# Kernel optimization log

Hardware: AMD Instinct MI355X
Metric: run time of the kernel (lower is better)

The kernel has to match this reference:

```python
import jax, jax.numpy as jnp
import numpy as np

# ---- static configuration (mirrors pdf.__init__ on a BaTiO3 system) ----
B, N = 2, 1024          # frames, atoms
NBINS = 100
R0, R1 = 0.5, 7.5       # r_range
CUTOFF = R1 + 0.5       # cutoff_boundary
L = 24.0                # cubic cell edge
PI = np.pi

# unique atomic numbers of BaTiO3, sorted (as __init__ computes from system.numbers)
UNIQUE_Z = [8, 22, 56]
ATOM_PAIRS = [(8, 8), (8, 22), (8, 56), (22, 22), (22, 56), (56, 56)]
_PAIR_COEFFI = {(82,82):125.44,(82,22):98.56,(82,8):107.52,(82,40):98.56,(56,56):125.44,
                (56,22):98.56,(56,8):107.52,(56,40):98.56,(22,22):19.36,(22,8):42.24,
                (22,40):19.36,(40,40):19.36,(40,8):42.24,(40,22):19.36,(8,8):23.04}
COEFFS = np.array([_PAIR_COEFFI.get(p, _PAIR_COEFFI.get((p[1], p[0]), 1.0))
                   for p in ATOM_PAIRS], dtype=np.float32)          # [T]
PAIR_KEYS = np.array([min(p)*1000 + max(p) for p in ATOM_PAIRS], dtype=np.int32)  # [T]

# static upper-triangular pair indices (i < j), as generate_nbr_list enumerates pairs once
I_IDX, J_IDX = np.triu_indices(N, k=1)   # each [P], P = N(N-1)/2


def setup_inputs() -> dict:
    key = jax.random.key(0)
    k1, _ = jax.random.split(key)
    xyz = jax.random.uniform(k1, (B, N, 3), dtype=jnp.float32) * L
    # BaTiO3 composition 1:1:3
    numbers = np.concatenate([np.full(205, 56), np.full(205, 22), np.full(614, 8)])
    rng = np.random.default_rng(0)
    rng.shuffle(numbers)
    bins = jnp.linspace(R0, R1, NBINS + 1, dtype=jnp.float32)
    cell = jnp.full((3,), L, dtype=jnp.float32)
    return {"xyz": xyz, "numbers": jnp.asarray(numbers, dtype=jnp.int32),
            "bins": bins, "cell": cell}


def reference(xyz, numbers, bins, cell):
    # per-pair unordered type key: min(z_i,z_j)*1000 + max(z_i,z_j)
    zi = numbers[I_IDX]
    zj = numbers[J_IDX]
    pair_key = jnp.minimum(zi, zj) * 1000 + jnp.maximum(zi, zj)          # [P]
    type_sel = (pair_key[None, :] == jnp.asarray(PAIR_KEYS)[:, None])    # [T, P] bool

    centers = 0.5 * (bins[:-1] + bins[1:])                               # [nbins]
    width = bins[1] - bins[0]
    sigma = width / np.sqrt(2.0 * PI)
    vol_bins = (4.0 * PI / 3.0) * (bins[1:] ** 3 - bins[:-1] ** 3)       # [nbins]
    V = (4.0 / 3.0) * PI * R1 ** 3
    coeffs = jnp.asarray(COEFFS)                                         # [T]

    def frame_pdf(x):                                                    # x: [N,3]
        d = x[I_IDX] - x[J_IDX]                                          # [P,3]
        d = d - cell * jnp.round(d / cell)                               # minimum image (diag cell)
        dist = jnp.sqrt(jnp.sum(d * d, axis=-1))                         # [P]
        within = dist < CUTOFF                                           # neighbor-list cutoff
        # Gaussian soft histogram kernel over all candidate pairs
        K = jnp.exp(-0.5 * ((dist[:, None] - centers[None, :]) / sigma) ** 2)  # [P,nbins]
        sel = (type_sel & within[None, :]).astype(K.dtype)               # [T,P]
        counts = sel @ K                                                 # [T,nbins]
        counts = counts / counts.sum(axis=-1, keepdims=True)
        rdf = counts / (vol_bins / V)[None, :]
        return jnp.sum(coeffs[:, None] * (rdf - 1.0), axis=0)            # [nbins]

    pdf_l = jax.vmap(frame_pdf)(xyz)                                     # [B,nbins]
    pdf_average = jnp.mean(pdf_l, axis=0) / 416.16
    return pdf_average, bins
```

## Files before the change

kernel.cpp:

```cpp
#include <hip/hip_runtime.h>
#include <math.h>

#define NBINS   100
#define NTYPES  6
#define NHIST   (NTYPES * NBINS)
#define NATOMS  1024
#define OPB     4
#define GPB     128
#define T1      1024
#define NW1     (T1 / 64)
#define R0f     0.5f
#define R1f     7.5f

__global__ __launch_bounds__(T1)
void pdf_pairs_rot(const float* __restrict__ xyz,
                   const int*   __restrict__ numbers,
                   const float* __restrict__ bins,
                   const float* __restrict__ cell,
                   float* __restrict__ partial,
                   float* __restrict__ out,
                   int out_size) {
    __shared__ float shist[NW1][NHIST];

    const int frame = blockIdx.y;
    const int tid   = threadIdx.x;
    const int wave  = tid >> 6;

    if (blockIdx.x == 0 && blockIdx.y == 0) {
        if (tid < NBINS) out[tid] = 0.0f;
        if (out_size >= NBINS + (NBINS + 1) && tid >= NBINS && tid < 2 * NBINS + 1)
            out[tid] = bins[tid - NBINS];
    }

    for (int k = tid; k < NW1 * NHIST; k += T1)
        ((float*)shist)[k] = 0.0f;

    const float* fx = xyz + (size_t)frame * NATOMS * 3;
    const float xi = fx[tid * 3 + 0];
    const float yi = fx[tid * 3 + 1];
    const float zi = fx[tid * 3 + 2];
    const int   zn = numbers[tid];
    const int   ti = (zn > 21) ? ((zn > 55) ? 2 : 1) : 0;

    const float cx = cell[0], cy = cell[1], cz = cell[2];
    const float icx = 1.0f / cx, icy = 1.0f / cy, icz = 1.0f / cz;
    const float w     = bins[1] - bins[0];
    const float sigma = w * 0.3989422804014327f;
    const float negc  = -(0.5f / (sigma * sigma)) * 1.4426950408889634f;
    const float invw  = 1.0f / w;
    const float w05   = 0.5f * w;
    const float c1    = -2.0f * negc * w;
    const float c2    = negc * w * w;

    __syncthreads();

    float* wh = shist[wave];

    #pragma unroll
    for (int q = 0; q < OPB; ++q) {
        const int o = blockIdx.x * OPB + 1 + q;
        const int j = (tid + o) & (NATOMS - 1);
        if (o == NATOMS / 2 && tid >= NATOMS / 2) continue;

        const float xj = fx[j * 3 + 0];
        const float yj = fx[j * 3 + 1];
        const float zj = fx[j * 3 + 2];
        const int   zjn = numbers[j];
        const int   tj = (zjn > 21) ? ((zjn > 55) ? 2 : 1) : 0;

        float dx = xi - xj;
        float dy = yi - yj;
        float dz = zi - zj;
        dx -= cx * rintf(dx * icx);
        dy -= cy * rintf(dy * icy);
        dz -= cz * rintf(dz * icz);
        const float dist = sqrtf(dx * dx + dy * dy + dz * dz);

        const int lo = min(ti, tj);
        const int hi = max(ti, tj);
        const int t  = 2 * lo - (lo >> 1) + hi;
        float* th = wh + t * NBINS;

        const float t0 = dist - R0f;
        const float kf = floorf(t0 * invw);
        const int   kc = (int)kf;
        const float base = (t0 - w05) - kf * w;
        const float A  = negc * base * base;
        const float Bq = c1 * base;

        #pragma unroll
        for (int u = 0; u < 5; ++u) {
            const float m = (float)(u - 2);
            const int   k = kc + (u - 2);
            const float arg = (A + m * m * c2) + m * Bq;
            const float v = __builtin_amdgcn_exp2f(arg);
            if ((unsigned)k < (unsigned)NBINS)
                atomicAdd(&th[k], v);
        }
    }
    __syncthreads();

    float* gp = partial + ((size_t)frame * GPB + blockIdx.x) * NHIST;
    for (int k = tid; k < NHIST; k += T1) {
        float v = 0.0f;
        #pragma unroll
        for (int wv = 0; wv < NW1; ++wv) v += shist[wv][k];
        gp[k] = v;
    }
}

__global__ __launch_bounds__(256)
void pdf_finish(const float* __restrict__ partial,
                const float* __restrict__ bins,
                float* __restrict__ out,
                int nframes) {
    __shared__ float wred[4];
    const int t   = blockIdx.x;
    const int b   = blockIdx.y;
    const int tid = threadIdx.x;

    float row = 0.0f;
    if (tid < NBINS) {
        const float* base = partial + (size_t)b * GPB * NHIST + t * NBINS + tid;
        #pragma unroll 8
        for (int g = 0; g < GPB; ++g)
            row += base[(size_t)g * NHIST];
    }

    float v = (tid < NBINS) ? row : 0.0f;
    #pragma unroll
    for (int off = 32; off > 0; off >>= 1) v += __shfl_down(v, off, 64);
    if ((tid & 63) == 0) wred[tid >> 6] = v;
    __syncthreads();
    const float ssum = (wred[0] + wred[1]) + (wred[2] + wred[3]);

    if (tid < NBINS) {
        const float PI = 3.14159265358979323846f;
        const float V = (4.0f / 3.0f) * PI * R1f * R1f * R1f;
        const float coeffs[NTYPES] = {23.04f, 42.24f, 107.52f, 19.36f, 98.56f, 125.44f};
        const float b0 = bins[tid], b1 = bins[tid + 1];
        const float volb = (4.0f * PI / 3.0f) * (b1 * b1 * b1 - b0 * b0 * b0);
        const float scale = V / volb;
        const float contrib = coeffs[t] * (row / ssum * scale - 1.0f)
                              / (float)nframes / 416.16f;
        unsafeAtomicAdd(&out[tid], contrib);
    }
}

extern "C" void kernel_launch(void* const* d_in, const int* in_sizes, int n_in,
                              void* d_out, int out_size, void* d_ws, size_t ws_size,
                              hipStream_t stream) {
    const float* xyz     = (const float*)d_in[0];
    const int*   numbers = (const int*)d_in[1];
    const float* bins    = (const float*)d_in[2];
    const float* cell    = (const float*)d_in[3];
    float* out     = (float*)d_out;
    float* partial = (float*)d_ws;

    const int B = in_sizes[0] / (NATOMS * 3);

    dim3 gridA(GPB, B);
    pdf_pairs_rot<<<gridA, T1, 0, stream>>>(xyz, numbers, bins, cell,
                                            partial, out, out_size);
    dim3 gridB(NTYPES, B);
    pdf_finish<<<gridB, 256, 0, stream>>>(partial, bins, out, B);
}
```

Before: 18.53 us.

## Halve block size with two atoms per thread, vectorize LDS, parallelize finish reduction

The pair kernel now uses 512-thread blocks, with each thread handling two i-atoms. The grid doubles to 256 blocks per frame with 2 offsets each, which halves the per-block LDS histogram footprint and raises the block count. Zeroing and reducing the LDS histograms now use float4 accesses. The finish kernel spreads the 256-partial sum over 1024 threads in 8 groups, then combines them through shared memory. The partial buffer gets twice as many rows, so there is more global write and read traffic in exchange for more parallelism.

```diff
diff --git a/kernel.cpp b/kernel.cpp
--- a/kernel.cpp
+++ b/kernel.cpp
@@ -5,9 +5,9 @@
 #define NTYPES  6
 #define NHIST   (NTYPES * NBINS)
 #define NATOMS  1024
-#define OPB     4
-#define GPB     128
-#define T1      1024
+#define OPB     2
+#define GPB     256
+#define T1      512
 #define NW1     (T1 / 64)
 #define R0f     0.5f
 #define R1f     7.5f
@@ -22,25 +22,29 @@
                    int out_size) {
     __shared__ float shist[NW1][NHIST];
 
-    const int frame = blockIdx.y;
     const int tid   = threadIdx.x;
     const int wave  = tid >> 6;
+    const int frame = blockIdx.y;
 
     if (blockIdx.x == 0 && blockIdx.y == 0) {
         if (tid < NBINS) out[tid] = 0.0f;
-        if (out_size >= NBINS + (NBINS + 1) && tid >= NBINS && tid < 2 * NBINS + 1)
+        if (out_size >= 2 * NBINS + 1 && tid >= NBINS && tid < 2 * NBINS + 1)
             out[tid] = bins[tid - NBINS];
     }
 
-    for (int k = tid; k < NW1 * NHIST; k += T1)
-        ((float*)shist)[k] = 0.0f;
+    {
+        float4* z = (float4*)&shist[0][0];
+        for (int v = tid; v < NW1 * NHIST / 4; v += T1)
+            z[v] = make_float4(0.f, 0.f, 0.f, 0.f);
+    }
 
     const float* fx = xyz + (size_t)frame * NATOMS * 3;
-    const float xi = fx[tid * 3 + 0];
-    const float yi = fx[tid * 3 + 1];
-    const float zi = fx[tid * 3 + 2];
-    const int   zn = numbers[tid];
-    const int   ti = (zn > 21) ? ((zn > 55) ? 2 : 1) : 0;
+    const int i0 = tid, i1 = tid + T1;
+    const float x0 = fx[i0 * 3 + 0], y0 = fx[i0 * 3 + 1], z0 = fx[i0 * 3 + 2];
+    const float x1 = fx[i1 * 3 + 0], y1 = fx[i1 * 3 + 1], z1 = fx[i1 * 3 + 2];
+    const int   zn0 = numbers[i0], zn1 = numbers[i1];
+    const int   t0i = (zn0 > 21) ? ((zn0 > 55) ? 2 : 1) : 0;
+    const int   t1i = (zn1 > 21) ? ((zn1 > 55) ? 2 : 1) : 0;
 
     const float cx = cell[0], cy = cell[1], cz = cell[2];
     const float icx = 1.0f / cx, icy = 1.0f / cy, icz = 1.0f / cz;
@@ -59,72 +63,96 @@
     #pragma unroll
     for (int q = 0; q < OPB; ++q) {
         const int o = blockIdx.x * OPB + 1 + q;
-        const int j = (tid + o) & (NATOMS - 1);
-        if (o == NATOMS / 2 && tid >= NATOMS / 2) continue;
-
-        const float xj = fx[j * 3 + 0];
-        const float yj = fx[j * 3 + 1];
-        const float zj = fx[j * 3 + 2];
-        const int   zjn = numbers[j];
-        const int   tj = (zjn > 21) ? ((zjn > 55) ? 2 : 1) : 0;
-
-        float dx = xi - xj;
-        float dy = yi - yj;
-        float dz = zi - zj;
-        dx -= cx * rintf(dx * icx);
-        dy -= cy * rintf(dy * icy);
-        dz -= cz * rintf(dz * icz);
-        const float dist = sqrtf(dx * dx + dy * dy + dz * dz);
-
-        const int lo = min(ti, tj);
-        const int hi = max(ti, tj);
-        const int t  = 2 * lo - (lo >> 1) + hi;
-        float* th = wh + t * NBINS;
-
-        const float t0 = dist - R0f;
-        const float kf = floorf(t0 * invw);
-        const int   kc = (int)kf;
-        const float base = (t0 - w05) - kf * w;
-        const float A  = negc * base * base;
-        const float Bq = c1 * base;
+        const bool do1 = (o != NATOMS / 2);
 
         #pragma unroll
-        for (int u = 0; u < 5; ++u) {
-            const float m = (float)(u - 2);
-            const int   k = kc + (u - 2);
-            const float arg = (A + m * m * c2) + m * Bq;
-            const float v = __builtin_amdgcn_exp2f(arg);
-            if ((unsigned)k < (unsigned)NBINS)
-                atomicAdd(&th[k], v);
+        for (int half = 0; half < 2; ++half) {
+            if (half == 1 && !do1) continue;
+            const int   i  = half ? i1 : i0;
+            const float xi = half ? x1 : x0;
+            const float yi = half ? y1 : y0;
+            const float zi = half ? z1 : z0;
+            const int   ti = half ? t1i : t0i;
+
+            const int j = (i + o) & (NATOMS - 1);
+            const float xj = fx[j * 3 + 0];
+            const float yj = fx[j * 3 + 1];
+            const float zj = fx[j * 3 + 2];
+            const int   zjn = numbers[j];
+            const int   tj = (zjn > 21) ? ((zjn > 55) ? 2 : 1) : 0;
+
+            float dx = xi - xj;
+            float dy = yi - yj;
+            float dz = zi - zj;
+            dx -= cx * rintf(dx * icx);
+            dy -= cy * rintf(dy * icy);
+            dz -= cz * rintf(dz * icz);
+            const float dist = sqrtf(dx * dx + dy * dy + dz * dz);
+
+            const int lo = min(ti, tj);
+            const int hi = max(ti, tj);
+            const int t  = 2 * lo - (lo >> 1) + hi;
+            float* th = wh + t * NBINS;
+
+            const float tt0 = dist - R0f;
+            const float kf  = floorf(tt0 * invw);
+            const int   kc  = (int)kf;
+            const float base = (tt0 - w05) - kf * w;
+            const float A  = negc * base * base;
+            const float Bq = c1 * base;
+
+            #pragma unroll
+            for (int u = 0; u < 5; ++u) {
+                const float m = (float)(u - 2);
+                const int   k = kc + (u - 2);
+                const float arg = (A + m * m * c2) + m * Bq;
+                const float v = __builtin_amdgcn_exp2f(arg);
+                if ((unsigned)k < (unsigned)NBINS)
+                    atomicAdd(&th[k], v);
+            }
         }
     }
     __syncthreads();
 
     float* gp = partial + ((size_t)frame * GPB + blockIdx.x) * NHIST;
-    for (int k = tid; k < NHIST; k += T1) {
-        float v = 0.0f;
+    if (tid < NHIST / 4) {
+        float4 acc = make_float4(0.f, 0.f, 0.f, 0.f);
         #pragma unroll
-        for (int wv = 0; wv < NW1; ++wv) v += shist[wv][k];
-        gp[k] = v;
+        for (int wv = 0; wv < NW1; ++wv) {
+            const float4 v = ((const float4*)shist[wv])[tid];
+            acc.x += v.x; acc.y += v.y; acc.z += v.z; acc.w += v.w;
+        }
+        ((float4*)gp)[tid] = acc;
     }
 }
 
-__global__ __launch_bounds__(256)
+__global__ __launch_bounds__(1024)
 void pdf_finish(const float* __restrict__ partial,
                 const float* __restrict__ bins,
                 float* __restrict__ out,
                 int nframes) {
-    __shared__ float wred[4];
+    __shared__ float rowpart[8][128];
+    __shared__ float wred[16];
     const int t   = blockIdx.x;
     const int b   = blockIdx.y;
     const int tid = threadIdx.x;
+    const int gg  = tid >> 7;
+    const int kk  = tid & 127;
+
+    float s = 0.0f;
+    if (kk < NBINS) {
+        const float* base = partial + (size_t)b * GPB * NHIST + t * NBINS + kk;
+        #pragma unroll 8
+        for (int g = gg; g < GPB; g += 8)
+            s += base[(size_t)g * NHIST];
+    }
+    rowpart[gg][kk] = s;
+    __syncthreads();
 
     float row = 0.0f;
     if (tid < NBINS) {
-        const float* base = partial + (size_t)b * GPB * NHIST + t * NBINS + tid;
-        #pragma unroll 8
-        for (int g = 0; g < GPB; ++g)
-            row += base[(size_t)g * NHIST];
+        #pragma unroll
+        for (int g = 0; g < 8; ++g) row += rowpart[g][tid];
     }
 
     float v = (tid < NBINS) ? row : 0.0f;
@@ -132,7 +160,7 @@
     for (int off = 32; off > 0; off >>= 1) v += __shfl_down(v, off, 64);
     if ((tid & 63) == 0) wred[tid >> 6] = v;
     __syncthreads();
-    const float ssum = (wred[0] + wred[1]) + (wred[2] + wred[3]);
+    const float ssum = wred[0] + wred[1];
 
     if (tid < NBINS) {
         const float PI = 3.14159265358979323846f;
@@ -163,5 +191,5 @@
     pdf_pairs_rot<<<gridA, T1, 0, stream>>>(xyz, numbers, bins, cell,
                                             partial, out, out_size);
     dim3 gridB(NTYPES, B);
-    pdf_finish<<<gridB, 256, 0, stream>>>(partial, bins, out, B);
+    pdf_finish<<<gridB, 1024, 0, stream>>>(partial, bins, out, B);
 }
```

After: 16.89 us. 8.9% less time.
